# Kernel tuning notes

Measured on AMD Instinct MI355X. Metric: run time of the kernel, lower is better.

## Reference

```python
import jax, jax.numpy as jnp
import numpy as np

B, N, D = 8, 256, 3          # batch, particles, spatial dims
H = 64                        # hidden_nf (channels)
L = 4                         # num_layers
ENC = 3                       # atom_type, aa_type, aa_pos
IN_NF = ENC + 1               # + time
COORDS_RANGE = 15.0 / L       # tanh=True -> coords_range/n_layers
E = B * N * N                 # fully-connected edges per batch graph


def _linear(key, fin, fout):
    k1, k2 = jax.random.split(key)
    s = 1.0 / np.sqrt(fin)
    w = jax.random.uniform(k1, (fout, fin), minval=-s, maxval=s, dtype=jnp.float32)
    b = jax.random.uniform(k2, (fout,), minval=-s, maxval=s, dtype=jnp.float32)
    return w, b


def setup_inputs() -> dict:
    key = jax.random.key(0)
    ks = jax.random.split(key, 64)
    inp = {
        "t": jax.random.uniform(ks[0], (B, 1), dtype=jnp.float32),
        "x": jax.random.normal(ks[1], (B, N * D), dtype=jnp.float32),
        "atom_type": jax.random.uniform(ks[2], (B, N), dtype=jnp.float32),
        "aa_type": jax.random.uniform(ks[3], (B, N), dtype=jnp.float32),
        "aa_pos": jax.random.uniform(ks[4], (B, N), dtype=jnp.float32),
        "node_mask": jnp.ones((B, N), dtype=jnp.float32),
    }
    inp["emb_w"], inp["emb_b"] = _linear(ks[5], IN_NF, H)
    specs = [("edge_w1", "edge_b1", 2 * H + 2, H), ("edge_w2", "edge_b2", H, H),
             ("node_w1", "node_b1", 2 * H, H), ("node_w2", "node_b2", H, H),
             ("coord_w1", "coord_b1", H, H), ("att_w", "att_b", H, 1)]
    kk = 6
    for wn, bn, fin, fout in specs:
        ws, bs = [], []
        for _ in range(L):
            w, b = _linear(ks[kk], fin, fout); kk += 1
            ws.append(w); bs.append(b)
        inp[wn] = jnp.stack(ws); inp[bn] = jnp.stack(bs)
    # final coord layer: Linear(H,1,bias=False), xavier gain 0.001
    inp["coord_w2"] = jax.random.normal(ks[kk], (L, 1, H), dtype=jnp.float32) * 0.001
    return inp


def _edges():
    idx = jnp.arange(N)
    row_in = jnp.repeat(idx, N)
    col_in = jnp.tile(idx, N)
    off = (jnp.arange(B) * N)[:, None]
    row = (off + row_in[None, :]).reshape(-1)
    col = (off + col_in[None, :]).reshape(-1)
    return row, col


def reference(t, x, atom_type, aa_type, aa_pos, node_mask,
              emb_w, emb_b, edge_w1, edge_b1, edge_w2, edge_b2,
              node_w1, node_b1, node_w2, node_b2,
              coord_w1, coord_b1, att_w, att_b, coord_w2):
    silu = jax.nn.silu
    row, col = _edges()
    nm = node_mask.reshape(B * N, 1)
    # edge mask: pairwise node mask with diagonal (self-loop) removed
    em = ((node_mask[:, :, None] * node_mask[:, None, :])
          * (1.0 - jnp.eye(N, dtype=jnp.float32))).reshape(E, 1)

    x0 = x.reshape(B * N, D) * nm
    tt = jnp.broadcast_to(t, (B, N)).reshape(B * N, 1) * nm
    h = jnp.stack([atom_type, aa_type, aa_pos], axis=-1).reshape(B * N, ENC) * nm
    h = jnp.concatenate([h, tt], axis=1)                      # [BN, 4]
    edge_attr0 = jnp.sum((x0[row] - x0[col]) ** 2, axis=1, keepdims=True)  # [E,1]

    h = h @ emb_w.T + emb_b                                   # embedding -> [BN, H]
    coord = x0
    for l in range(L):
        diff = coord[row] - coord[col]                        # [E, D]
        radial = jnp.sum(diff ** 2, axis=1, keepdims=True)    # [E, 1]
        diff = diff / (jnp.sqrt(radial + 1e-8) + 1.0)         # norm_diff
        m = jnp.concatenate([h[row], h[col], radial, edge_attr0], axis=1)
        m = silu(m @ edge_w1[l].T + edge_b1[l])
        m = silu(m @ edge_w2[l].T + edge_b2[l])               # [E, H]
        m = m * jax.nn.sigmoid(m @ att_w[l].T + att_b[l]) * em
        phi = jnp.tanh(silu(m @ coord_w1[l].T + coord_b1[l]) @ coord_w2[l].T)
        trans = diff * phi * COORDS_RANGE * em                # [E, D]
        coord = (coord + jax.ops.segment_sum(trans, row, num_segments=B * N)) * nm
        agg = jax.ops.segment_sum(m, row, num_segments=B * N)  # [BN, H]
        upd = jnp.concatenate([h, agg], axis=1)
        upd = silu(upd @ node_w1[l].T + node_b1[l]) @ node_w2[l].T + node_b2[l]
        h = (h + upd) * nm                                    # recurrent residual

    vel = (coord - x0) * nm
    vel = vel.reshape(B, N, D)
    nmr = node_mask.reshape(B, N, 1)
    Ns = jnp.sum(nmr, axis=1, keepdims=True)
    vel = vel - (jnp.sum(vel, axis=1, keepdims=True) / Ns) * nmr  # remove_mean_with_mask
    return vel.reshape(B, N * D)
```

## Files before the change

kernel.cpp:

```cpp
#include <hip/hip_runtime.h>

#define CRANGE 3.75f

typedef _Float16 half_t;
typedef __attribute__((ext_vector_type(8))) _Float16 half8;
typedef __attribute__((ext_vector_type(4))) _Float16 half4;
typedef __attribute__((ext_vector_type(4))) float f32x4;

__device__ __forceinline__ float frcp(float x) { return __builtin_amdgcn_rcpf(x); }
__device__ __forceinline__ float fexpn(float x) { return __expf(fminf(x, 20.f)); }
__device__ __forceinline__ float fsilu(float x) { return x * frcp(1.f + fexpn(-x)); }

__device__ __forceinline__ void inv4(float d0, float d1, float d2, float d3, float* o) {
    float p01 = d0 * d1, p23 = d2 * d3;
    float r = frcp(p01 * p23);
    float t01 = p23 * r, t23 = p01 * r;
    o[0] = d1 * t01; o[1] = d0 * t01; o[2] = d3 * t23; o[3] = d2 * t23;
}
__device__ __forceinline__ void silu4(const float* x, float* o) {
    float d0 = 1.f + fexpn(-x[0]), d1 = 1.f + fexpn(-x[1]);
    float d2 = 1.f + fexpn(-x[2]), d3 = 1.f + fexpn(-x[3]);
    float iv[4]; inv4(d0, d1, d2, d3, iv);
    o[0] = x[0] * iv[0]; o[1] = x[1] * iv[1]; o[2] = x[2] * iv[2]; o[3] = x[3] * iv[3];
}

__global__ __launch_bounds__(256) void k_prepinit(
    const float* __restrict__ ew2, const float* __restrict__ cw1,
    const float* __restrict__ nw1, const float* __restrict__ nw2,
    const float* __restrict__ ew1,
    half_t* __restrict__ wf, float* __restrict__ trT,
    const float* __restrict__ t, const float* __restrict__ x,
    const float* __restrict__ at, const float* __restrict__ aa,
    const float* __restrict__ ap, const float* __restrict__ nm,
    const float* __restrict__ embw, const float* __restrict__ embb,
    const float* __restrict__ eb1_0,
    float* __restrict__ h, float* __restrict__ Hr, float* __restrict__ HcA,
    float* __restrict__ x0, float* __restrict__ cA)
{
    if (blockIdx.x < 336) {
        int idx = blockIdx.x * 256 + threadIdx.x;
        if (idx < 4096) {
            int lane = idx & 63;
            int g = (idx >> 6) & 7;
            int mat = (idx >> 9) & 1;
            int l = idx >> 10;
            int mt = g >> 1, kc = g & 1;
            int c = lane & 15, qq = lane >> 4;
            const float* W = (mat ? cw1 : ew2) + l * 4096;
            int row = 16 * mt + c;
            int k0 = 32 * kc + 8 * qq;
            half8 pk;
#pragma unroll
            for (int j = 0; j < 8; ++j) pk[j] = (half_t)W[row * 64 + k0 + j];
            ((half8*)wf)[idx] = pk;
        }
        int tid2 = idx - 4096;
        if (tid2 >= 0 && tid2 < 81920) {
            int l = tid2 / 20480, r = tid2 % 20480;
            float v;
            if (r < 8192)       { int k = r >> 6,        c = r & 63; v = nw1[l * 8192 + c * 128 + k]; }
            else if (r < 12288) { int r2 = r - 8192,  k = r2 >> 6, c = r2 & 63; v = nw2[l * 4096 + c * 64 + k]; }
            else if (r < 16384) { int r2 = r - 12288, k = r2 >> 6, c = r2 & 63; v = ew1[l * 8320 + c * 130 + k]; }
            else                { int r2 = r - 16384, k = r2 >> 6, c = r2 & 63; v = ew1[l * 8320 + c * 130 + 64 + k]; }
            trT[l * 20480 + r] = v;
        }
        return;
    }
    __shared__ float sh[4][64];
    int g = threadIdx.x >> 6, c = threadIdx.x & 63;
    int n = (blockIdx.x - 336) * 4 + g;
    float m = nm[n]; int b = n >> 8;
    float i0 = at[n] * m, i1 = aa[n] * m, i2 = ap[n] * m, i3 = t[b] * m;
    float4 w = ((const float4*)embw)[c];
    float hv = w.x * i0 + w.y * i1 + w.z * i2 + w.w * i3 + embb[c];
    sh[g][c] = hv; h[n * 64 + c] = hv;
    if (c < 3) { float v = x[n * 3 + c] * m; x0[n * 3 + c] = v; cA[n * 3 + c] = v; }
    __syncthreads();
    float a = eb1_0[c], bb = 0.f;
    const float* wa = ew1 + c * 130;
#pragma unroll
    for (int k = 0; k < 64; ++k) {
        float hk = sh[g][k];
        a  += wa[k] * hk;
        bb += wa[64 + k] * hk;
    }
    Hr[n * 64 + c] = a;
    HcA[n * 64 + c] = bb;
}

__global__ __launch_bounds__(256, 4) void k_edge(
    const float* __restrict__ coordIn, const float* __restrict__ x0,
    float* __restrict__ Hr, const float* __restrict__ Hc,
    const float* __restrict__ ew1, const float* __restrict__ eb2,
    const float* __restrict__ cb1, const float* __restrict__ attw,
    const float* __restrict__ attb, const float* __restrict__ cw2,
    const float* __restrict__ nm, const half_t* __restrict__ wf2,
    const half_t* __restrict__ wf1,
    float* __restrict__ hbuf,
    const float* __restrict__ nw1T, const float* __restrict__ nw2T,
    const float* __restrict__ nb1, const float* __restrict__ nb2,
    const float* __restrict__ ew1aTn, const float* __restrict__ ew1bTn,
    const float* __restrict__ eb1n,
    float* __restrict__ HcO, float* __restrict__ coordOut)
{
    __shared__ __align__(16) half_t sV[4][4096];
    __shared__ __align__(16) float sGeo[4][64][4];
    __shared__ float sHr[64], sWr[64], sWe[64], sB2[64], sBc1[64], sAttw[64], sWc2[64];
    __shared__ float sAgg[64];
    __shared__ float sCoord[3];

    const int i = blockIdx.x, b = i >> 8, ir = i & 255;
    const int t = threadIdx.x, wv = t >> 6, e = t & 63;
    const int q = e >> 4, c = e & 15;
    const int col = (b << 8) + t;

    if (t < 64) {
        sHr[t] = Hr[i * 64 + t];
        sWr[t] = ew1[t * 130 + 128];
        sWe[t] = ew1[t * 130 + 129];
        sB2[t] = eb2[t]; sBc1[t] = cb1[t]; sAttw[t] = attw[t]; sWc2[t] = cw2[t];
        sAgg[t] = 0.f;
    }
    if (t == 64) { sCoord[0] = 0.f; sCoord[1] = 0.f; sCoord[2] = 0.f; }
    float attb0 = attb[0];
    float nmi = nm[i];

    float dx = coordIn[i*3+0] - coordIn[col*3+0];
    float dy = coordIn[i*3+1] - coordIn[col*3+1];
    float dz = coordIn[i*3+2] - coordIn[col*3+2];
    float radial = dx*dx + dy*dy + dz*dz;
    float inv = frcp(__builtin_amdgcn_sqrtf(radial + 1e-8f) + 1.f);
    float ex = x0[i*3+0] - x0[col*3+0];
    float ey = x0[i*3+1] - x0[col*3+1];
    float ez = x0[i*3+2] - x0[col*3+2];
    float e0 = ex*ex + ey*ey + ez*ez;
    float em = nmi * nm[col] * ((t == ir) ? 0.f : 1.f);

    __syncthreads();

    {
        float4 g4 = make_float4(dx*inv, dy*inv, dz*inv, em);
        *(float4*)&sGeo[wv][e][0] = g4;
    }

    half_t* mybuf = (half_t*)sV[wv];
    const float4* hcv = (const float4*)(Hc + col * 64);
#pragma unroll
    for (int s = 0; s < 8; ++s) {
        float4 ha = hcv[2*s], hb = hcv[2*s+1];
        float z[8], so[8];
        z[0]=ha.x; z[1]=ha.y; z[2]=ha.z; z[3]=ha.w;
        z[4]=hb.x; z[5]=hb.y; z[6]=hb.z; z[7]=hb.w;
#pragma unroll
        for (int u = 0; u < 8; ++u) {
            int k = 8*s + u;
            z[u] = sHr[k] + z[u] + radial * sWr[k] + e0 * sWe[k];
        }
        silu4(z, so); silu4(z + 4, so + 4);
        half8 pk;
#pragma unroll
        for (int u = 0; u < 8; ++u) pk[u] = (half_t)so[u];
        int f = q * 2 + (s >> 2);
        *(half8*)&mybuf[f * 512 + ((s & 3) * 16 + c) * 8] = pk;
    }

    const half8* bv = (const half8*)mybuf;
    f32x4 acc[4][4];
#pragma unroll
    for (int mt = 0; mt < 4; ++mt) {
        int row0 = 16*mt + 4*q;
#pragma unroll
        for (int nt = 0; nt < 4; ++nt)
#pragma unroll
            for (int r = 0; r < 4; ++r) acc[mt][nt][r] = sB2[row0 + r];
    }
    {
        const half8* a2v = (const half8*)wf2;
        half8 a2[8];
#pragma unroll
        for (int g = 0; g < 8; ++g) a2[g] = a2v[g * 64 + e];
#pragma unroll
        for (int nt = 0; nt < 4; ++nt) {
            half8 b0 = bv[(nt*2+0)*64 + e];
            half8 b1 = bv[(nt*2+1)*64 + e];
#pragma unroll
            for (int mt = 0; mt < 4; ++mt) {
                acc[mt][nt] = __builtin_amdgcn_mfma_f32_16x16x32_f16(a2[mt*2+0], b0, acc[mt][nt], 0, 0, 0);
                acc[mt][nt] = __builtin_amdgcn_mfma_f32_16x16x32_f16(a2[mt*2+1], b1, acc[mt][nt], 0, 0, 0);
            }
        }
    }

    float attp[4] = {0.f, 0.f, 0.f, 0.f};
#pragma unroll
    for (int mt = 0; mt < 4; ++mt) {
        int row0 = 16*mt + 4*q;
#pragma unroll
        for (int nt = 0; nt < 4; ++nt) {
            float z[4], so[4];
#pragma unroll
            for (int r = 0; r < 4; ++r) z[r] = acc[mt][nt][r];
            silu4(z, so);
#pragma unroll
            for (int r = 0; r < 4; ++r) {
                acc[mt][nt][r] = so[r];
                attp[nt] += so[r] * sAttw[row0 + r];
            }
        }
    }
#pragma unroll
    for (int nt = 0; nt < 4; ++nt) {
        float v = attp[nt];
        v += __shfl_xor(v, 16);
        v += __shfl_xor(v, 32);
        attp[nt] = v;
    }
    float scale[4];
    {
        float d0 = 1.f + fexpn(-(attp[0] + attb0));
        float d1 = 1.f + fexpn(-(attp[1] + attb0));
        float d2 = 1.f + fexpn(-(attp[2] + attb0));
        float d3 = 1.f + fexpn(-(attp[3] + attb0));
        float iv[4]; inv4(d0, d1, d2, d3, iv);
#pragma unroll
        for (int nt = 0; nt < 4; ++nt) scale[nt] = iv[nt] * sGeo[wv][16*nt + c][3];
    }

    float aggp[4][4];
#pragma unroll
    for (int mt = 0; mt < 4; ++mt)
#pragma unroll
        for (int r = 0; r < 4; ++r) aggp[mt][r] = 0.f;
#pragma unroll
    for (int mt = 0; mt < 4; ++mt) {
        int kbase = 16*mt + 4*q;
        int fof = ((kbase >> 5) * 512) + (((kbase >> 3) & 3) * 128) + (kbase & 7);
#pragma unroll
        for (int nt = 0; nt < 4; ++nt) {
            half4 pk;
#pragma unroll
            for (int r = 0; r < 4; ++r) {
                float v = acc[mt][nt][r] * scale[nt];
                aggp[mt][r] += v;
                pk[r] = (half_t)v;
            }
            *(half4*)&mybuf[nt*1024 + fof + c*8] = pk;
        }
    }

    half8 a1[8];
    {
        const half8* a1v = (const half8*)wf1;
#pragma unroll
        for (int g = 0; g < 8; ++g) a1[g] = a1v[g * 64 + e];
    }

#pragma unroll
    for (int mt = 0; mt < 4; ++mt)
#pragma unroll
        for (int r = 0; r < 4; ++r) {
            float v = aggp[mt][r];
            v += __shfl_xor(v, 1); v += __shfl_xor(v, 2);
            v += __shfl_xor(v, 4); v += __shfl_xor(v, 8);
            if (c == 0) atomicAdd(&sAgg[16*mt + 4*q + r], v);
        }

    f32x4 acc2[4][4];
#pragma unroll
    for (int mt = 0; mt < 4; ++mt) {
        int row0 = 16*mt + 4*q;
#pragma unroll
        for (int nt = 0; nt < 4; ++nt)
#pragma unroll
            for (int r = 0; r < 4; ++r) acc2[mt][nt][r] = sBc1[row0 + r];
    }
#pragma unroll
    for (int nt = 0; nt < 4; ++nt) {
        half8 b0 = bv[(nt*2+0)*64 + e];
        half8 b1 = bv[(nt*2+1)*64 + e];
#pragma unroll
        for (int mt = 0; mt < 4; ++mt) {
            acc2[mt][nt] = __builtin_amdgcn_mfma_f32_16x16x32_f16(a1[mt*2+0], b0, acc2[mt][nt], 0, 0, 0);
            acc2[mt][nt] = __builtin_amdgcn_mfma_f32_16x16x32_f16(a1[mt*2+1], b1, acc2[mt][nt], 0, 0, 0);
        }
    }

    float php[4] = {0.f, 0.f, 0.f, 0.f};
#pragma unroll
    for (int mt = 0; mt < 4; ++mt) {
        int row0 = 16*mt + 4*q;
#pragma unroll
        for (int nt = 0; nt < 4; ++nt) {
            float z[4], so[4];
#pragma unroll
            for (int r = 0; r < 4; ++r) z[r] = acc2[mt][nt][r];
            silu4(z, so);
#pragma unroll
            for (int r = 0; r < 4; ++r) php[nt] += so[r] * sWc2[row0 + r];
        }
    }
#pragma unroll
    for (int nt = 0; nt < 4; ++nt) {
        float v = php[nt];
        v += __shfl_xor(v, 16);
        v += __shfl_xor(v, 32);
        php[nt] = v;
    }
    float tnh[4];
    {
        float d0 = fexpn(2.f * php[0]) + 1.f;
        float d1 = fexpn(2.f * php[1]) + 1.f;
        float d2 = fexpn(2.f * php[2]) + 1.f;
        float d3 = fexpn(2.f * php[3]) + 1.f;
        float iv[4]; inv4(d0, d1, d2, d3, iv);
#pragma unroll
        for (int nt = 0; nt < 4; ++nt) tnh[nt] = 1.f - 2.f * iv[nt];
    }
    float tx = 0.f, ty = 0.f, tz = 0.f;
#pragma unroll
    for (int nt = 0; nt < 4; ++nt) {
        float4 g4 = *(float4*)&sGeo[wv][16*nt + c][0];
        float tr = tnh[nt] * CRANGE * g4.w;
        tx += g4.x * tr; ty += g4.y * tr; tz += g4.z * tr;
    }
    tx += __shfl_xor(tx, 1); tx += __shfl_xor(tx, 2); tx += __shfl_xor(tx, 4); tx += __shfl_xor(tx, 8);
    ty += __shfl_xor(ty, 1); ty += __shfl_xor(ty, 2); ty += __shfl_xor(ty, 4); ty += __shfl_xor(ty, 8);
    tz += __shfl_xor(tz, 1); tz += __shfl_xor(tz, 2); tz += __shfl_xor(tz, 4); tz += __shfl_xor(tz, 8);
    if (e == 0) {
        atomicAdd(&sCoord[0], tx);
        atomicAdd(&sCoord[1], ty);
        atomicAdd(&sCoord[2], tz);
    }

    __syncthreads();

    float* sT  = (float*)&sV[0][0];
    float* sIn = sT;
    float* sU  = sT + 128;
    float* sHn = sT + 192;

    if (t < 64) sIn[t] = hbuf[i * 64 + t];
    else if (t < 128) sIn[t] = sAgg[t - 64];
    if (t >= 128 && t < 131) {
        int d = t - 128;
        coordOut[i * 3 + d] = (coordIn[i * 3 + d] + sCoord[d]) * nmi;
    }
    __syncthreads();

    const int o = (wv << 4) + c;
    {
        float a = 0.f;
        const float* w = nw1T + (q * 32) * 64 + o;
#pragma unroll
        for (int k = 0; k < 32; ++k) a += w[k * 64] * sIn[q * 32 + k];
        a += __shfl_xor(a, 16);
        a += __shfl_xor(a, 32);
        if (q == 0) sU[o] = fsilu(a + nb1[o]);
    }
    __syncthreads();
    {
        float a = 0.f;
        const float* w = nw2T + (q * 16) * 64 + o;
#pragma unroll
        for (int k = 0; k < 16; ++k) a += w[k * 64] * sU[q * 16 + k];
        a += __shfl_xor(a, 16);
        a += __shfl_xor(a, 32);
        if (q == 0) {
            float hn = (sIn[o] + a + nb2[o]) * nmi;
            hbuf[i * 64 + o] = hn;
            sHn[o] = hn;
        }
    }
    __syncthreads();
    {
        float a = 0.f, bb = 0.f;
        const float* wa = ew1aTn + (q * 16) * 64 + o;
        const float* wb = ew1bTn + (q * 16) * 64 + o;
#pragma unroll
        for (int k = 0; k < 16; ++k) {
            float hv = sHn[q * 16 + k];
            a  += wa[k * 64] * hv;
            bb += wb[k * 64] * hv;
        }
        a  += __shfl_xor(a, 16);  a  += __shfl_xor(a, 32);
        bb += __shfl_xor(bb, 16); bb += __shfl_xor(bb, 32);
        if (q == 0) {
            Hr[i * 64 + o]  = a + eb1n[o];
            HcO[i * 64 + o] = bb;
        }
    }
}

__global__ void k_final(const float* __restrict__ coord, const float* __restrict__ x0,
                        const float* __restrict__ nm, float* __restrict__ out) {
    int b = blockIdx.x;
    int t = threadIdx.x;
    int i = b * 256 + t;
    int lane = t & 63;
    float m = nm[i];
    float vx = (coord[i * 3 + 0] - x0[i * 3 + 0]) * m;
    float vy = (coord[i * 3 + 1] - x0[i * 3 + 1]) * m;
    float vz = (coord[i * 3 + 2] - x0[i * 3 + 2]) * m;
    __shared__ float red[4];
    if (t < 4) red[t] = 0.f;
    __syncthreads();
    float sx = vx, sy = vy, sz = vz, sn = m;
#pragma unroll
    for (int off = 1; off < 64; off <<= 1) {
        sx += __shfl_xor(sx, off);
        sy += __shfl_xor(sy, off);
        sz += __shfl_xor(sz, off);
        sn += __shfl_xor(sn, off);
    }
    if (lane == 0) {
        atomicAdd(&red[0], sx); atomicAdd(&red[1], sy);
        atomicAdd(&red[2], sz); atomicAdd(&red[3], sn);
    }
    __syncthreads();
    float invNs = frcp(red[3]);
    out[b * 768 + t * 3 + 0] = vx - red[0] * invNs * m;
    out[b * 768 + t * 3 + 1] = vy - red[1] * invNs * m;
    out[b * 768 + t * 3 + 2] = vz - red[2] * invNs * m;
}

extern "C" void kernel_launch(void* const* d_in, const int* in_sizes, int n_in,
                              void* d_out, int out_size, void* d_ws, size_t ws_size,
                              hipStream_t stream) {
    const float* t_in    = (const float*)d_in[0];
    const float* x_in    = (const float*)d_in[1];
    const float* at_in   = (const float*)d_in[2];
    const float* aa_in   = (const float*)d_in[3];
    const float* ap_in   = (const float*)d_in[4];
    const float* nm_in   = (const float*)d_in[5];
    const float* emb_w   = (const float*)d_in[6];
    const float* emb_b   = (const float*)d_in[7];
    const float* edge_w1 = (const float*)d_in[8];
    const float* edge_b1 = (const float*)d_in[9];
    const float* edge_w2 = (const float*)d_in[10];
    const float* edge_b2 = (const float*)d_in[11];
    const float* node_w1 = (const float*)d_in[12];
    const float* node_b1 = (const float*)d_in[13];
    const float* node_w2 = (const float*)d_in[14];
    const float* node_b2 = (const float*)d_in[15];
    const float* coord_w1= (const float*)d_in[16];
    const float* coord_b1= (const float*)d_in[17];
    const float* att_w   = (const float*)d_in[18];
    const float* att_b   = (const float*)d_in[19];
    const float* coord_w2= (const float*)d_in[20];

    float* ws  = (float*)d_ws;
    float* h   = ws;
    float* Hr  = h + 131072;
    float* HcA = Hr + 131072;
    float* HcB = HcA + 131072;
    float* x0  = HcB + 131072;
    float* cA  = x0 + 6144;
    float* cB  = cA + 6144;
    float* base = cB + 6144;
    half_t* wf = (half_t*)base;
    float* trT = base + 16384;

    float* out = (float*)d_out;

    k_prepinit<<<848, 256, 0, stream>>>(edge_w2, coord_w1, node_w1, node_w2, edge_w1,
                                        wf, trT,
                                        t_in, x_in, at_in, aa_in, ap_in, nm_in,
                                        emb_w, emb_b, edge_b1,
                                        h, Hr, HcA, x0, cA);

    for (int l = 0; l < 4; ++l) {
        const float* ew1 = edge_w1 + l * 8320;
        const float* eb2 = edge_b2 + l * 64;
        const float* cb1 = coord_b1 + l * 64;
        const float* aw  = att_w + l * 64;
        const float* ab  = att_b + l;
        const float* cw2 = coord_w2 + l * 64;
        const float* nb1 = node_b1 + l * 64;
        const float* nb2 = node_b2 + l * 64;

        const float* trL = trT + l * 20480;
        int ln = (l + 1) & 3;
        const float* trN = trT + ln * 20480;

        const float* cin  = (l & 1) ? cB : cA;
        float*       cout = (l & 1) ? cA : cB;
        const float* HcR  = (l & 1) ? HcB : HcA;
        float*       HcW  = (l & 1) ? HcA : HcB;

        k_edge<<<2048, 256, 0, stream>>>(cin, x0, Hr, HcR, ew1, eb2, cb1,
                                         aw, ab, cw2, nm_in,
                                         wf + l * 8192, wf + l * 8192 + 4096,
                                         h, trL, trL + 8192, nb1, nb2,
                                         trN + 12288, trN + 16384, edge_b1 + ln * 64,
                                         HcW, cout);
    }

    k_final<<<8, 256, 0, stream>>>(cA, x0, nm_in, out);
}
```

Baseline: 309.6 us.

## Split node update into separate MFMA tail kernel per layer

Moves the per-node MLP update (node_w1, node_w2, and the next layer's edge_w1 projections) out of the tail of each edge block into a new k_tail kernel. That kernel processes 64 nodes per block with fp16 MFMA, and the weights are pre-packed into fragment layout in the prep kernel. The edge kernel now writes the aggregated messages to a global buffer and drops its serial scalar matvecs, which lowers register and LDS pressure (launch bounds change to 3 waves). The cost is an extra launch per layer and a global round-trip for agg. The agg input is split into fp16 hi/lo parts to keep its precision, while h and the intermediate activations are rounded to fp16.

Result: no change. 308.8 us (-0.3%).

```diff
diff --git a/kernel.cpp b/kernel.cpp
--- a/kernel.cpp
+++ b/kernel.cpp
@@ -28,47 +28,74 @@
     const float* __restrict__ ew2, const float* __restrict__ cw1,
     const float* __restrict__ nw1, const float* __restrict__ nw2,
     const float* __restrict__ ew1,
-    half_t* __restrict__ wf, float* __restrict__ trT,
+    half_t* __restrict__ wf, half_t* __restrict__ wfT,
     const float* __restrict__ t, const float* __restrict__ x,
     const float* __restrict__ at, const float* __restrict__ aa,
     const float* __restrict__ ap, const float* __restrict__ nm,
     const float* __restrict__ embw, const float* __restrict__ embb,
     const float* __restrict__ eb1_0,
-    float* __restrict__ h, float* __restrict__ Hr, float* __restrict__ HcA,
+    float* __restrict__ h, float* __restrict__ Hr, float* __restrict__ Hc,
     float* __restrict__ x0, float* __restrict__ cA)
 {
-    if (blockIdx.x < 336) {
+    if (blockIdx.x < 16) {
         int idx = blockIdx.x * 256 + threadIdx.x;
-        if (idx < 4096) {
-            int lane = idx & 63;
-            int g = (idx >> 6) & 7;
-            int mat = (idx >> 9) & 1;
-            int l = idx >> 10;
-            int mt = g >> 1, kc = g & 1;
-            int c = lane & 15, qq = lane >> 4;
-            const float* W = (mat ? cw1 : ew2) + l * 4096;
+        int lane = idx & 63;
+        int g = (idx >> 6) & 7;
+        int mat = (idx >> 9) & 1;
+        int l = idx >> 10;
+        int mt = g >> 1, kc = g & 1;
+        int c = lane & 15, qq = lane >> 4;
+        const float* W = (mat ? cw1 : ew2) + l * 4096;
+        int row = 16 * mt + c;
+        int k0 = 32 * kc + 8 * qq;
+        half8 pk;
+#pragma unroll
+        for (int j = 0; j < 8; ++j) pk[j] = (half_t)W[row * 64 + k0 + j];
+        ((half8*)wf)[idx] = pk;
+        return;
+    }
+    if (blockIdx.x < 64) {
+        int idx = (blockIdx.x - 16) * 256 + threadIdx.x;
+        int l = idx / 3072, r = idx % 3072;
+        int lane = r & 63;
+        int c = lane & 15, qq = lane >> 4;
+        half8 pk;
+        if (r < 1536) {
+            int f = r >> 6;
+            int kc = f >> 2, mt = f & 3;
             int row = 16 * mt + c;
             int k0 = 32 * kc + 8 * qq;
-            half8 pk;
-#pragma unroll
-            for (int j = 0; j < 8; ++j) pk[j] = (half_t)W[row * 64 + k0 + j];
-            ((half8*)wf)[idx] = pk;
-        }
-        int tid2 = idx - 4096;
-        if (tid2 >= 0 && tid2 < 81920) {
-            int l = tid2 / 20480, r = tid2 % 20480;
-            float v;
-            if (r < 8192)       { int k = r >> 6,        c = r & 63; v = nw1[l * 8192 + c * 128 + k]; }
-            else if (r < 12288) { int r2 = r - 8192,  k = r2 >> 6, c = r2 & 63; v = nw2[l * 4096 + c * 64 + k]; }
-            else if (r < 16384) { int r2 = r - 12288, k = r2 >> 6, c = r2 & 63; v = ew1[l * 8320 + c * 130 + k]; }
-            else                { int r2 = r - 16384, k = r2 >> 6, c = r2 & 63; v = ew1[l * 8320 + c * 130 + 64 + k]; }
-            trT[l * 20480 + r] = v;
-        }
+            const float* src = nw1 + l * 8192 + row * 128;
+#pragma unroll
+            for (int j = 0; j < 8; ++j) {
+                int k = k0 + j;
+                pk[j] = (half_t)src[(k < 128) ? k : (k - 64)];
+            }
+        } else if (r < 2048) {
+            int f = (r - 1536) >> 6;
+            int kc = f >> 2, mt = f & 3;
+            const float* src = nw2 + l * 4096 + (16 * mt + c) * 64 + 32 * kc + 8 * qq;
+#pragma unroll
+            for (int j = 0; j < 8; ++j) pk[j] = (half_t)src[j];
+        } else if (r < 2560) {
+            int f = (r - 2048) >> 6;
+            int kc = f >> 2, mt = f & 3;
+            const float* src = ew1 + l * 8320 + (16 * mt + c) * 130 + 32 * kc + 8 * qq;
+#pragma unroll
+            for (int j = 0; j < 8; ++j) pk[j] = (half_t)src[j];
+        } else {
+            int f = (r - 2560) >> 6;
+            int kc = f >> 2, mt = f & 3;
+            const float* src = ew1 + l * 8320 + (16 * mt + c) * 130 + 64 + 32 * kc + 8 * qq;
+#pragma unroll
+            for (int j = 0; j < 8; ++j) pk[j] = (half_t)src[j];
+        }
+        ((half8*)wfT)[idx] = pk;
         return;
     }
     __shared__ float sh[4][64];
     int g = threadIdx.x >> 6, c = threadIdx.x & 63;
-    int n = (blockIdx.x - 336) * 4 + g;
+    int n = (blockIdx.x - 64) * 4 + g;
     float m = nm[n]; int b = n >> 8;
     float i0 = at[n] * m, i1 = aa[n] * m, i2 = ap[n] * m, i3 = t[b] * m;
     float4 w = ((const float4*)embw)[c];
@@ -85,23 +112,18 @@
         bb += wa[64 + k] * hk;
     }
     Hr[n * 64 + c] = a;
-    HcA[n * 64 + c] = bb;
+    Hc[n * 64 + c] = bb;
 }
 
-__global__ __launch_bounds__(256, 4) void k_edge(
+__global__ __launch_bounds__(256, 3) void k_edge(
     const float* __restrict__ coordIn, const float* __restrict__ x0,
-    float* __restrict__ Hr, const float* __restrict__ Hc,
+    const float* __restrict__ Hr, const float* __restrict__ Hc,
     const float* __restrict__ ew1, const float* __restrict__ eb2,
     const float* __restrict__ cb1, const float* __restrict__ attw,
     const float* __restrict__ attb, const float* __restrict__ cw2,
     const float* __restrict__ nm, const half_t* __restrict__ wf2,
     const half_t* __restrict__ wf1,
-    float* __restrict__ hbuf,
-    const float* __restrict__ nw1T, const float* __restrict__ nw2T,
-    const float* __restrict__ nb1, const float* __restrict__ nb2,
-    const float* __restrict__ ew1aTn, const float* __restrict__ ew1bTn,
-    const float* __restrict__ eb1n,
-    float* __restrict__ HcO, float* __restrict__ coordOut)
+    float* __restrict__ coordOut, float* __restrict__ aggO)
 {
     __shared__ __align__(16) half_t sV[4][4096];
     __shared__ __align__(16) float sGeo[4][64][4];
@@ -333,60 +355,151 @@
     }
 
     __syncthreads();
-
-    float* sT  = (float*)&sV[0][0];
-    float* sIn = sT;
-    float* sU  = sT + 128;
-    float* sHn = sT + 192;
-
-    if (t < 64) sIn[t] = hbuf[i * 64 + t];
-    else if (t < 128) sIn[t] = sAgg[t - 64];
-    if (t >= 128 && t < 131) {
-        int d = t - 128;
+    if (t < 64) aggO[i * 64 + t] = sAgg[t];
+    if (t >= 64 && t < 67) {
+        int d = t - 64;
         coordOut[i * 3 + d] = (coordIn[i * 3 + d] + sCoord[d]) * nmi;
     }
-    __syncthreads();
-
-    const int o = (wv << 4) + c;
-    {
-        float a = 0.f;
-        const float* w = nw1T + (q * 32) * 64 + o;
-#pragma unroll
-        for (int k = 0; k < 32; ++k) a += w[k * 64] * sIn[q * 32 + k];
-        a += __shfl_xor(a, 16);
-        a += __shfl_xor(a, 32);
-        if (q == 0) sU[o] = fsilu(a + nb1[o]);
-    }
-    __syncthreads();
-    {
-        float a = 0.f;
-        const float* w = nw2T + (q * 16) * 64 + o;
-#pragma unroll
-        for (int k = 0; k < 16; ++k) a += w[k * 64] * sU[q * 16 + k];
-        a += __shfl_xor(a, 16);
-        a += __shfl_xor(a, 32);
-        if (q == 0) {
-            float hn = (sIn[o] + a + nb2[o]) * nmi;
-            hbuf[i * 64 + o] = hn;
-            sHn[o] = hn;
-        }
-    }
-    __syncthreads();
-    {
-        float a = 0.f, bb = 0.f;
-        const float* wa = ew1aTn + (q * 16) * 64 + o;
-        const float* wb = ew1bTn + (q * 16) * 64 + o;
-#pragma unroll
-        for (int k = 0; k < 16; ++k) {
-            float hv = sHn[q * 16 + k];
-            a  += wa[k * 64] * hv;
-            bb += wb[k * 64] * hv;
-        }
-        a  += __shfl_xor(a, 16);  a  += __shfl_xor(a, 32);
-        bb += __shfl_xor(bb, 16); bb += __shfl_xor(bb, 32);
-        if (q == 0) {
-            Hr[i * 64 + o]  = a + eb1n[o];
-            HcO[i * 64 + o] = bb;
+}
+
+__global__ __launch_bounds__(256, 2) void k_tail(
+    float* __restrict__ hbuf, const float* __restrict__ agg, const float* __restrict__ nm,
+    const half_t* __restrict__ wfn,
+    const half_t* __restrict__ wfe,
+    const float* __restrict__ nb1, const float* __restrict__ nb2,
+    const float* __restrict__ eb1n,
+    float* __restrict__ Hr, float* __restrict__ Hc)
+{
+    __shared__ __align__(16) half_t sBF[12288];
+    __shared__ __align__(16) half_t sUF[4096];
+    __shared__ __align__(16) half_t sHF[4096];
+
+    const int n0 = blockIdx.x * 64;
+    const int t = threadIdx.x, w = t >> 6, L = t & 63;
+    const int q = L >> 4, c = L & 15;
+    const int row0 = 16 * w + 4 * q;
+
+    const half8* wn1  = (const half8*)wfn;
+    const half8* wn2  = ((const half8*)wfn) + 1536;
+    const half8* we1a = ((const half8*)wfe) + 2048;
+    const half8* we1b = ((const half8*)wfe) + 2560;
+
+#pragma unroll
+    for (int r5 = 0; r5 < 6; ++r5) {
+        int idx = r5 * 256 + t;
+        int node = idx & 63, oct = idx >> 6;
+        int kc = oct >> 2, qq = oct & 3;
+        int nt = node >> 4, cc = node & 15;
+        int g = n0 + node;
+        half8 pk;
+        if (kc < 2) {
+            const float* src = hbuf + g * 64 + kc * 32 + qq * 8;
+#pragma unroll
+            for (int j = 0; j < 8; ++j) pk[j] = (half_t)src[j];
+        } else if (kc < 4) {
+            const float* src = agg + g * 64 + (kc - 2) * 32 + qq * 8;
+#pragma unroll
+            for (int j = 0; j < 8; ++j) pk[j] = (half_t)src[j];
+        } else {
+            const float* src = agg + g * 64 + (kc - 4) * 32 + qq * 8;
+#pragma unroll
+            for (int j = 0; j < 8; ++j) {
+                float a = src[j];
+                half_t hi = (half_t)a;
+                pk[j] = (half_t)(a - (float)hi);
+            }
+        }
+        *(half8*)&sBF[((nt * 6 + kc) * 64 + (qq * 16 + cc)) * 8] = pk;
+    }
+    __syncthreads();
+
+    half8 a[6];
+#pragma unroll
+    for (int kc = 0; kc < 6; ++kc) a[kc] = wn1[(kc * 4 + w) * 64 + L];
+    const half8* bIn = (const half8*)sBF;
+    f32x4 acc[4];
+#pragma unroll
+    for (int nt = 0; nt < 4; ++nt)
+#pragma unroll
+        for (int r = 0; r < 4; ++r) acc[nt][r] = nb1[row0 + r];
+#pragma unroll
+    for (int nt = 0; nt < 4; ++nt)
+#pragma unroll
+        for (int kc = 0; kc < 6; ++kc)
+            acc[nt] = __builtin_amdgcn_mfma_f32_16x16x32_f16(a[kc], bIn[(nt * 6 + kc) * 64 + L], acc[nt], 0, 0, 0);
+
+    const int fof = ((row0 >> 5) * 512) + (((row0 >> 3) & 3) * 128) + (row0 & 7);
+#pragma unroll
+    for (int nt = 0; nt < 4; ++nt) {
+        float z[4], so[4];
+#pragma unroll
+        for (int r = 0; r < 4; ++r) z[r] = acc[nt][r];
+        silu4(z, so);
+        half4 pk;
+#pragma unroll
+        for (int r = 0; r < 4; ++r) pk[r] = (half_t)so[r];
+        *(half4*)&sUF[nt * 1024 + fof + c * 8] = pk;
+    }
+    __syncthreads();
+
+    half8 a2[2];
+#pragma unroll
+    for (int kc = 0; kc < 2; ++kc) a2[kc] = wn2[(kc * 4 + w) * 64 + L];
+    const half8* bU = (const half8*)sUF;
+    f32x4 acc2[4];
+#pragma unroll
+    for (int nt = 0; nt < 4; ++nt)
+#pragma unroll
+        for (int r = 0; r < 4; ++r) acc2[nt][r] = nb2[row0 + r];
+#pragma unroll
+    for (int nt = 0; nt < 4; ++nt)
+#pragma unroll
+        for (int kc = 0; kc < 2; ++kc)
+            acc2[nt] = __builtin_amdgcn_mfma_f32_16x16x32_f16(a2[kc], bU[(nt * 2 + kc) * 64 + L], acc2[nt], 0, 0, 0);
+
+#pragma unroll
+    for (int nt = 0; nt < 4; ++nt) {
+        int g = n0 + 16 * nt + c;
+        float mnode = nm[g];
+        float* hp = hbuf + g * 64 + row0;
+        half4 pk;
+#pragma unroll
+        for (int r = 0; r < 4; ++r) {
+            float hn = (hp[r] + acc2[nt][r]) * mnode;
+            hp[r] = hn;
+            pk[r] = (half_t)hn;
+        }
+        *(half4*)&sHF[nt * 1024 + fof + c * 8] = pk;
+    }
+    __syncthreads();
+
+    half8 ea[2], eb[2];
+#pragma unroll
+    for (int kc = 0; kc < 2; ++kc) {
+        ea[kc] = we1a[(kc * 4 + w) * 64 + L];
+        eb[kc] = we1b[(kc * 4 + w) * 64 + L];
+    }
+    const half8* bH = (const half8*)sHF;
+    f32x4 acc3[4], acc4[4];
+#pragma unroll
+    for (int nt = 0; nt < 4; ++nt)
+#pragma unroll
+        for (int r = 0; r < 4; ++r) { acc3[nt][r] = eb1n[row0 + r]; acc4[nt][r] = 0.f; }
+#pragma unroll
+    for (int nt = 0; nt < 4; ++nt)
+#pragma unroll
+        for (int kc = 0; kc < 2; ++kc) {
+            half8 bh = bH[(nt * 2 + kc) * 64 + L];
+            acc3[nt] = __builtin_amdgcn_mfma_f32_16x16x32_f16(ea[kc], bh, acc3[nt], 0, 0, 0);
+            acc4[nt] = __builtin_amdgcn_mfma_f32_16x16x32_f16(eb[kc], bh, acc4[nt], 0, 0, 0);
+        }
+#pragma unroll
+    for (int nt = 0; nt < 4; ++nt) {
+        int g = n0 + 16 * nt + c;
+#pragma unroll
+        for (int r = 0; r < 4; ++r) {
+            Hr[g * 64 + row0 + r] = acc3[nt][r];
+            Hc[g * 64 + row0 + r] = acc4[nt][r];
         }
     }
 }
@@ -451,22 +564,22 @@
     float* ws  = (float*)d_ws;
     float* h   = ws;
     float* Hr  = h + 131072;
-    float* HcA = Hr + 131072;
-    float* HcB = HcA + 131072;
-    float* x0  = HcB + 131072;
+    float* Hc  = Hr + 131072;
+    float* agg = Hc + 131072;
+    float* x0  = agg + 131072;
     float* cA  = x0 + 6144;
     float* cB  = cA + 6144;
     float* base = cB + 6144;
-    half_t* wf = (half_t*)base;
-    float* trT = base + 16384;
+    half_t* wf  = (half_t*)base;
+    half_t* wfT = (half_t*)(base + 16384);
 
     float* out = (float*)d_out;
 
-    k_prepinit<<<848, 256, 0, stream>>>(edge_w2, coord_w1, node_w1, node_w2, edge_w1,
-                                        wf, trT,
+    k_prepinit<<<576, 256, 0, stream>>>(edge_w2, coord_w1, node_w1, node_w2, edge_w1,
+                                        wf, wfT,
                                         t_in, x_in, at_in, aa_in, ap_in, nm_in,
                                         emb_w, emb_b, edge_b1,
-                                        h, Hr, HcA, x0, cA);
+                                        h, Hr, Hc, x0, cA);
 
     for (int l = 0; l < 4; ++l) {
         const float* ew1 = edge_w1 + l * 8320;
@@ -475,24 +588,22 @@
         const float* aw  = att_w + l * 64;
         const float* ab  = att_b + l;
         const float* cw2 = coord_w2 + l * 64;
-        const float* nb1 = node_b1 + l * 64;
-        const float* nb2 = node_b2 + l * 64;
-
-        const float* trL = trT + l * 20480;
-        int ln = (l + 1) & 3;
-        const float* trN = trT + ln * 20480;
 
         const float* cin  = (l & 1) ? cB : cA;
         float*       cout = (l & 1) ? cA : cB;
-        const float* HcR  = (l & 1) ? HcB : HcA;
-        float*       HcW  = (l & 1) ? HcA : HcB;
-
-        k_edge<<<2048, 256, 0, stream>>>(cin, x0, Hr, HcR, ew1, eb2, cb1,
+
+        k_edge<<<2048, 256, 0, stream>>>(cin, x0, Hr, Hc, ew1, eb2, cb1,
                                          aw, ab, cw2, nm_in,
                                          wf + l * 8192, wf + l * 8192 + 4096,
-                                         h, trL, trL + 8192, nb1, nb2,
-                                         trN + 12288, trN + 16384, edge_b1 + ln * 64,
-                                         HcW, cout);
+                                         cout, agg);
+        if (l < 3) {
+            int ln = l + 1;
+            k_tail<<<32, 256, 0, stream>>>(h, agg, nm_in,
+                                           wfT + l * 24576, wfT + ln * 24576,
+                                           node_b1 + l * 64, node_b2 + l * 64,
+                                           edge_b1 + ln * 64,
+                                           Hr, Hc);
+        }
     }
 
     k_final<<<8, 256, 0, stream>>>(cA, x0, nm_in, out);
```
